# Performance work log

Measured on AMD Instinct MI355X. Metric: run time of the kernel, lower is better.

The kernel has to match this reference:

```python
import jax, jax.numpy as jnp
import numpy as np

NUM_HEADS = 12


def setup_inputs() -> dict:
    key = jax.random.key(0)
    ks = jax.random.split(key, 6)
    B, N, C = 2, 1569, 768  # N = 1 + num_frames * seq_len = 1 + 8*196
    s = 0.02
    return {
        "x": jax.random.normal(ks[0], (B, N, C), jnp.float32),
        "W_qkv": jax.random.normal(ks[1], (C, 3 * C), jnp.float32) * s,
        "W_pq": jax.random.normal(ks[2], (C, C), jnp.float32) * s,
        "W_pkv": jax.random.normal(ks[3], (C, 2 * C), jnp.float32) * s,
        "W_proj": jax.random.normal(ks[4], (C, C), jnp.float32) * s,
        "b_proj": jax.random.normal(ks[5], (C,), jnp.float32) * s,
        "seq_len": 196,
        "num_frames": 8,
    }


def reference(x, W_qkv, W_pq, W_pkv, W_proj, b_proj, seq_len, num_frames):
    h = NUM_HEADS
    B, N, C = x.shape
    d = C // h
    P, F = seq_len, num_frames  # N == 1 + F*P
    S = F * P
    scale = d ** (-0.5)

    # qkv projection (no bias), split heads -> (B*h, N, d)
    qkv = x @ W_qkv
    q, k, v = jnp.split(qkv, 3, axis=-1)

    def heads(t):
        return t.reshape(B, N, h, d).transpose(0, 2, 1, 3).reshape(B * h, N, d)

    q, k, v = map(heads, (q, k, v))

    # --- CLS token: plain attention over all tokens ---
    cls_sim = jnp.einsum('bid,bjd->bij', q[:, :1] * scale, k)  # (B*h,1,N)
    cls_attn = jax.nn.softmax(cls_sim, axis=-1)
    cls_out = jnp.einsum('bij,bjd->bid', cls_attn, v)  # (B*h,1,d)
    cls_out = cls_out.reshape(B, h, 1, d).transpose(0, 2, 1, 3).reshape(B, 1, C)

    # --- Stage 1: space attention (softmax over patches n within each frame f) ---
    q_, k_, v_ = q[:, 1:], k[:, 1:], v[:, 1:]  # (B*h, S, d)
    q_dot_k = jnp.einsum('bqd,bnd->bqn', q_, k_).reshape(B * h, S, F, P)
    space_attn = jax.nn.softmax(scale * q_dot_k, axis=-1)  # (B*h, S, F, P)
    v4 = v_.reshape(B * h, F, P, d)
    traj = jnp.einsum('bqfn,bfnd->bqfd', space_attn, v4)  # (B*h, S, F, d)
    # merge heads into channels: (B, S, F, C)
    traj = traj.reshape(B, h, S, F, d).transpose(0, 2, 3, 1, 4).reshape(B, S, F, C)

    # --- Diagonal gather: token s=f*P+n takes its own-frame trajectory f ---
    fidx = jnp.repeat(jnp.arange(F), P)  # (S,)
    x_diag = jnp.take_along_axis(traj, fidx[None, :, None, None], axis=2)[:, :, 0, :]  # (B,S,C)

    # --- Stage 2: temporal attention over frames f ---
    q2 = (x_diag @ W_pq).reshape(B, S, h, d).transpose(0, 2, 1, 3) * scale  # (B,h,S,d)
    kv2 = traj @ W_pkv  # (B,S,F,2C)
    k2, v2 = jnp.split(kv2, 2, axis=-1)

    def heads5(t):  # (B,S,F,C) -> (B,h,S,F,d)
        return t.reshape(B, S, F, h, d).transpose(0, 3, 1, 2, 4)

    k2 = heads5(k2)
    attn = jax.nn.softmax(jnp.einsum('bhsd,bhsfd->bhsf', q2, k2), axis=-1)  # (B,h,S,F)
    # use_original_code=True: values are the trajectory tensor itself, not v2
    xv = heads5(traj)
    out = jnp.einsum('bhsf,bhsfd->bhsd', attn, xv)  # (B,h,S,d)
    out = out.transpose(0, 2, 1, 3).reshape(B, S, C)

    out = jnp.concatenate([cls_out, out], axis=1) @ W_proj + b_proj  # (B,N,C)
    return out, attn
```

## Files before the change

### kernel.cpp

```cpp
#include <hip/hip_runtime.h>

#define B_ 2
#define N_ 1569
#define C_ 768
#define H_ 12
#define D_ 64
#define P_ 196
#define F_ 8
#define S_ 1568
#define QKVLD 2304
#define SCALE 0.125f

typedef unsigned short ushort_t;
using short8 = __attribute__((ext_vector_type(8))) short;
using f32x4  = __attribute__((ext_vector_type(4))) float;

__device__ __forceinline__ ushort_t f2bf(float x) {
    unsigned u = __float_as_uint(x);
    u += 0x7fffu + ((u >> 16) & 1);
    return (ushort_t)(u >> 16);
}
__device__ __forceinline__ float bf2f(ushort_t h) {
    return __uint_as_float((unsigned)h << 16);
}
__device__ __forceinline__ uint2 pack4(float a, float b, float c, float d) {
    uint2 o;
    o.x = f2bf(a) | ((unsigned)f2bf(b) << 16);
    o.y = f2bf(c) | ((unsigned)f2bf(d) << 16);
    return o;
}

__global__ __launch_bounds__(256)
void cvt_f32_bf16(const float* __restrict__ s, ushort_t* __restrict__ d, int n4)
{
    int i = blockIdx.x * 256 + threadIdx.x;
    if (i < n4) {
        float4 v = ((const float4*)s)[i];
        ((uint2*)d)[i] = pack4(v.x, v.y, v.z, v.w);
    }
}

__global__ __launch_bounds__(256)
void transpose_cvt(const float* __restrict__ src, ushort_t* __restrict__ dst,
                   int K, int ldsrc)
{
    __shared__ float tle[32][33];
    const int n0 = blockIdx.x * 32, k0 = blockIdx.y * 32;
    const int tx = threadIdx.x & 31, ty = threadIdx.x >> 5;
#pragma unroll
    for (int j = 0; j < 4; j++)
        tle[ty + 8 * j][tx] = src[(long)(k0 + ty + 8 * j) * ldsrc + n0 + tx];
    __syncthreads();
#pragma unroll
    for (int j = 0; j < 4; j++)
        dst[(long)(n0 + ty + 8 * j) * K + k0 + tx] = f2bf(tle[tx][ty + 8 * j]);
}

template<int GATHER, int OUTBF>
__global__ __launch_bounds__(256)
void gemm_bf16(const ushort_t* __restrict__ A, const ushort_t* __restrict__ Bt,
               void* __restrict__ Cv, int M, int Nn, int K,
               float alpha, const float* __restrict__ bias)
{
    __shared__ ushort_t As[128][32];
    __shared__ ushort_t Bs[128][32];

    const int tid = threadIdx.x;

    const int nwg = gridDim.x;
    const int GY  = Nn >> 7;
    const int bid = blockIdx.x;
    const int qch = nwg >> 3, rch = nwg & 7;
    const int xcd = bid & 7, lidx = bid >> 3;
    const int wg = (xcd < rch ? xcd * (qch + 1)
                              : rch * (qch + 1) + (xcd - rch) * qch) + lidx;
    const int m0 = (wg / GY) * 128, n0 = (wg % GY) * 128;

    const int wave = tid >> 6, lane = tid & 63;
    const int wm = (wave & 1) * 64, wn = (wave >> 1) * 64;
    const int lrow = lane & 15, quad = lane >> 4;

    const int srow = tid >> 2, sseg = tid & 3;
    const int wseg = sseg ^ ((srow >> 1) & 3);
    int ma0 = m0 + srow;      if (ma0 >= M) ma0 = M - 1;
    int ma1 = m0 + 64 + srow; if (ma1 >= M) ma1 = M - 1;
    long ra0, ra1;
    if (GATHER) {
        ra0 = (long)ma0 * F_ + (ma0 % S_) / P_;
        ra1 = (long)ma1 * F_ + (ma1 % S_) / P_;
    } else { ra0 = ma0; ra1 = ma1; }
    const ushort_t* ap0 = A + ra0 * K + sseg * 8;
    const ushort_t* ap1 = A + ra1 * K + sseg * 8;
    const ushort_t* bp0 = Bt + (long)(n0 + srow) * K + sseg * 8;
    const ushort_t* bp1 = Bt + (long)(n0 + 64 + srow) * K + sseg * 8;

    f32x4 acc[4][4];
#pragma unroll
    for (int i = 0; i < 4; i++)
#pragma unroll
        for (int j = 0; j < 4; j++) acc[i][j] = (f32x4){0.f, 0.f, 0.f, 0.f};

    const int rchunk = (quad ^ ((lrow >> 1) & 3)) * 8;

    uint4 aV0 = *(const uint4*)ap0;
    uint4 aV1 = *(const uint4*)ap1;
    uint4 bV0 = *(const uint4*)bp0;
    uint4 bV1 = *(const uint4*)bp1;

    const int nk = K >> 5;
    for (int kt = 0; kt < nk; kt++) {
        __syncthreads();
        *(uint4*)&As[srow][wseg * 8]      = aV0;
        *(uint4*)&As[64 + srow][wseg * 8] = aV1;
        *(uint4*)&Bs[srow][wseg * 8]      = bV0;
        *(uint4*)&Bs[64 + srow][wseg * 8] = bV1;
        __syncthreads();
        if (kt + 1 < nk) {
            int k0 = (kt + 1) * 32;
            aV0 = *(const uint4*)(ap0 + k0);
            aV1 = *(const uint4*)(ap1 + k0);
            bV0 = *(const uint4*)(bp0 + k0);
            bV1 = *(const uint4*)(bp1 + k0);
        }
        short8 af[4], bf[4];
#pragma unroll
        for (int mt = 0; mt < 4; mt++)
            af[mt] = *(const short8*)&As[wm + mt * 16 + lrow][rchunk];
#pragma unroll
        for (int nt = 0; nt < 4; nt++)
            bf[nt] = *(const short8*)&Bs[wn + nt * 16 + lrow][rchunk];
#pragma unroll
        for (int mt = 0; mt < 4; mt++)
#pragma unroll
            for (int nt = 0; nt < 4; nt++)
                acc[mt][nt] = __builtin_amdgcn_mfma_f32_16x16x32_bf16(
                    af[mt], bf[nt], acc[mt][nt], 0, 0, 0);
    }

#pragma unroll
    for (int mt = 0; mt < 4; mt++) {
#pragma unroll
        for (int nt = 0; nt < 4; nt++) {
            int row = m0 + wm + mt * 16 + quad * 4;
            int col = n0 + wn + nt * 16 + lrow;
            float bv = bias ? bias[col] : 0.f;
#pragma unroll
            for (int r = 0; r < 4; r++) {
                if (row + r < M) {
                    float v = acc[mt][nt][r] * alpha + bv;
                    if (OUTBF)
                        ((ushort_t*)Cv)[(long)(row + r) * Nn + col] = f2bf(v);
                    else
                        ((float*)Cv)[(long)(row + r) * Nn + col] = v;
                }
            }
        }
    }
}

__global__ __launch_bounds__(256)
void prep_kv(const float* __restrict__ qkv, ushort_t* __restrict__ q_bf,
             ushort_t* __restrict__ k_bf, ushort_t* __restrict__ vT_bf)
{
    const int f = blockIdx.x, h = blockIdx.y, b = blockIdx.z;
    const int t = threadIdx.x;
    const long rowbase = (long)(b * N_ + 1 + f * P_) * QKVLD;

    {
        ushort_t* qd = q_bf + ((long)(b * H_ + h) * S_ + f * P_) * 64;
        for (int u = t; u < P_ * 16; u += 256) {
            int row = u >> 4, seg = u & 15;
            float4 v = *(const float4*)(qkv + rowbase + (long)row * QKVLD + h * 64 + seg * 4);
            *(uint2*)(qd + (long)row * 64 + seg * 4) = pack4(v.x, v.y, v.z, v.w);
        }
    }
    {
        ushort_t* kd = k_bf + (long)((b * H_ + h) * F_ + f) * 13312;
        for (int u = t; u < 208 * 16; u += 256) {
            int key = u >> 4, seg = u & 15;
            float4 v = make_float4(0.f, 0.f, 0.f, 0.f);
            if (key < P_)
                v = *(const float4*)(qkv + rowbase + (long)key * QKVLD + 768 + h * 64 + seg * 4);
            int ks = seg >> 3, qq = (seg >> 1) & 3, j0 = (seg & 1) * 4;
            int nt = key >> 4, lr = key & 15;
            *(uint2*)(kd + ((ks * 13 + nt) * 64 + qq * 16 + lr) * 8 + j0)
                = pack4(v.x, v.y, v.z, v.w);
        }
    }
    __shared__ float Vl[224][68];
    for (int u = t; u < 224 * 16; u += 256) {
        int key = u >> 4, seg = u & 15;
        float4 v = make_float4(0.f, 0.f, 0.f, 0.f);
        if (key < P_)
            v = *(const float4*)(qkv + rowbase + (long)key * QKVLD + 1536 + h * 64 + seg * 4);
        *(float4*)&Vl[key][seg * 4] = v;
    }
    __syncthreads();
    {
        ushort_t* vd = vT_bf + (long)((b * H_ + h) * F_ + f) * 14336;
        for (int u = t; u < 64 * 56; u += 256) {
            int d = u / 56, kb = u % 56;
            int s = kb >> 3, qq = (kb >> 1) & 3, j0 = (kb & 1) * 4;
            int nt = d >> 4, lr = d & 15;
            *(uint2*)(vd + ((s * 4 + nt) * 64 + qq * 16 + lr) * 8 + j0) =
                pack4(Vl[kb*4+0][d], Vl[kb*4+1][d], Vl[kb*4+2][d], Vl[kb*4+3][d]);
        }
    }
}

__global__ __launch_bounds__(256)
void traj_attn_mfma(const ushort_t* __restrict__ q_bf,
                    const ushort_t* __restrict__ k_bf,
                    const ushort_t* __restrict__ vT_bf,
                    ushort_t* __restrict__ traj)
{
    __shared__ __align__(16) ushort_t Pl[4][7 * 512];

    const int t = threadIdx.x;
    const int wave = t >> 6, lane = t & 63;
    const int lrow = lane & 15, quad = lane >> 4;
    const int qt = blockIdx.x, h = blockIdx.y, b = blockIdx.z;
    const int s0 = qt * 64;
    const bool v12 = (lrow < 4);

    int qrow = s0 + wave * 16 + lrow; if (qrow > S_ - 1) qrow = S_ - 1;
    const ushort_t* qp = q_bf + ((long)(b * H_ + h) * S_ + qrow) * 64 + quad * 8;
    short8 a0 = *(const short8*)qp;
    short8 a1 = *(const short8*)(qp + 32);

    *(uint2*)&Pl[wave][6 * 512 + 256 + lane * 4] = (uint2){0, 0};

    const ushort_t* kfb = k_bf  + (long)((b * H_ + h) * F_) * 13312;
    const ushort_t* vfb = vT_bf + (long)((b * H_ + h) * F_) * 14336;

#pragma unroll 1
    for (int f = 0; f < F_; f++) {
        const ushort_t* kf = kfb + (long)f * 13312;
        const ushort_t* vf = vfb + (long)f * 14336;

        f32x4 acc[13];
#pragma unroll
        for (int nt = 0; nt < 13; nt++) acc[nt] = (f32x4){0.f, 0.f, 0.f, 0.f};
#pragma unroll
        for (int nt = 0; nt < 13; nt++) {
            short8 bv = *(const short8*)(kf + (long)nt * 512 + lane * 8);
            acc[nt] = __builtin_amdgcn_mfma_f32_16x16x32_bf16(a0, bv, acc[nt], 0, 0, 0);
        }
#pragma unroll
        for (int nt = 0; nt < 13; nt++) {
            short8 bv = *(const short8*)(kf + (long)(13 + nt) * 512 + lane * 8);
            acc[nt] = __builtin_amdgcn_mfma_f32_16x16x32_bf16(a1, bv, acc[nt], 0, 0, 0);
        }

        float rl[4];
#pragma unroll
        for (int r = 0; r < 4; r++) {
            float mx = acc[0][r];
#pragma unroll
            for (int nt = 1; nt < 12; nt++) mx = fmaxf(mx, acc[nt][r]);
            if (v12) mx = fmaxf(mx, acc[12][r]);
#pragma unroll
            for (int off = 1; off < 16; off <<= 1)
                mx = fmaxf(mx, __shfl_xor(mx, off, 16));
            float sum = 0.f;
#pragma unroll
            for (int nt = 0; nt < 12; nt++) {
                float w = __expf((acc[nt][r] - mx) * SCALE);
                acc[nt][r] = w; sum += w;
            }
            {
                float w = v12 ? __expf((acc[12][r] - mx) * SCALE) : 0.f;
                acc[12][r] = w; sum += w;
            }
#pragma unroll
            for (int off = 1; off < 16; off <<= 1)
                sum += __shfl_xor(sum, off, 16);
            rl[r] = 1.f / sum;
        }

#pragma unroll
        for (int nt = 0; nt < 13; nt++) {
            int key = nt * 16 + lrow;
            int base = (key >> 5) * 512 + ((key >> 3) & 3) * 128 + (key & 7) + quad * 32;
#pragma unroll
            for (int r = 0; r < 4; r++)
                Pl[wave][base + r * 8] = f2bf(acc[nt][r]);
        }
        asm volatile("s_waitcnt lgkmcnt(0)" ::: "memory");

        f32x4 av[4];
#pragma unroll
        for (int nt = 0; nt < 4; nt++) av[nt] = (f32x4){0.f, 0.f, 0.f, 0.f};
#pragma unroll
        for (int s = 0; s < 7; s++) {
            short8 af = *(const short8*)&Pl[wave][s * 512 + lane * 8];
#pragma unroll
            for (int nt = 0; nt < 4; nt++) {
                short8 bv = *(const short8*)(vf + (long)(s * 4 + nt) * 512 + lane * 8);
                av[nt] = __builtin_amdgcn_mfma_f32_16x16x32_bf16(af, bv, av[nt], 0, 0, 0);
            }
        }

#pragma unroll
        for (int nt = 0; nt < 4; nt++)
#pragma unroll
            for (int r = 0; r < 4; r++) {
                int so = s0 + wave * 16 + quad * 4 + r;
                if (so < S_)
                    traj[((long)(b * S_ + so) * F_ + f) * C_ + h * 64 + nt * 16 + lrow]
                        = f2bf(av[nt][r] * rl[r]);
            }
    }
}

#define CLS_CH 13
__global__ __launch_bounds__(256)
void cls_attn_part(const float* __restrict__ qkv, float* __restrict__ part)
{
    const int c = blockIdx.x, hh = blockIdx.y, b = blockIdx.z;
    const int t = threadIdx.x;
    const int n0 = c * 128;
    const int nk = (N_ - n0 < 128) ? (N_ - n0) : 128;

    __shared__ float qs[64];
    __shared__ float sc[128];
    __shared__ float red[256];

    if (t < 64) qs[t] = qkv[(long)(b * N_) * QKVLD + hh * 64 + t];
    __syncthreads();

    if (t < 128) {
        float acc = -1e30f;
        if (t < nk) {
            const float* krow = qkv + (long)(b * N_ + n0 + t) * QKVLD + 768 + hh * 64;
            acc = 0.f;
#pragma unroll
            for (int j4 = 0; j4 < 16; j4++) {
                float4 kv = *(const float4*)(krow + j4 * 4);
                acc = fmaf(kv.x, qs[j4*4+0], acc);
                acc = fmaf(kv.y, qs[j4*4+1], acc);
                acc = fmaf(kv.z, qs[j4*4+2], acc);
                acc = fmaf(kv.w, qs[j4*4+3], acc);
            }
            acc *= SCALE;
        }
        sc[t] = acc;
        red[t] = acc;
    }
    __syncthreads();
    for (int s = 64; s > 0; s >>= 1) {
        if (t < s && t + s < 128) red[t] = fmaxf(red[t], red[t + s]);
        __syncthreads();
    }
    const float m = red[0];
    __syncthreads();

    if (t < 128) {
        float w = (t < nk) ? __expf(sc[t] - m) : 0.f;
        sc[t] = w;
        red[t] = w;
    }
    __syncthreads();
    for (int s = 64; s > 0; s >>= 1) {
        if (t < s && t + s < 128) red[t] += red[t + s];
        __syncthreads();
    }
    const float lsum = red[0];
    __syncthreads();

    const int j = t & 63, grp = t >> 6;
    float acc = 0.f;
    for (int n = grp; n < nk; n += 4)
        acc = fmaf(sc[n], qkv[(long)(b * N_ + n0 + n) * QKVLD + 1536 + hh * 64 + j], acc);
    red[t] = acc;
    __syncthreads();

    float* pp = part + (long)(((b * H_ + hh) * CLS_CH) + c) * 68;
    if (t < 64)
        pp[2 + t] = red[t] + red[64 + t] + red[128 + t] + red[192 + t];
    if (t == 0) { pp[0] = m; pp[1] = lsum; }
}

__global__ __launch_bounds__(64)
void cls_attn_merge(const float* __restrict__ part, float* __restrict__ outcat)
{
    const int bh = blockIdx.x;
    const int b = bh / H_, hh = bh % H_;
    const int t = threadIdx.x;
    const float* pp = part + (long)(bh * CLS_CH) * 68;

    float m = -1e30f;
#pragma unroll
    for (int c = 0; c < CLS_CH; c++) m = fmaxf(m, pp[c * 68]);
    float l = 0.f, o = 0.f;
#pragma unroll
    for (int c = 0; c < CLS_CH; c++) {
        float w = __expf(pp[c * 68] - m);
        l = fmaf(pp[c * 68 + 1], w, l);
        o = fmaf(pp[c * 68 + 2 + t], w, o);
    }
    outcat[(long)(b * N_) * C_ + hh * 64 + t] = o / l;
}

__global__ __launch_bounds__(256)
void attn2_kernel(const float* __restrict__ q2, const ushort_t* __restrict__ k2,
                  const ushort_t* __restrict__ traj, float* __restrict__ outcat,
                  float* __restrict__ attn_out)
{
    const int bs = blockIdx.x;
    const int b = bs / S_, s = bs % S_;
    __shared__ float qs[768];
    __shared__ ushort_t ks[8 * 768];
    __shared__ float logit[12][8];
    __shared__ float wsm[12][8];
    const int t = threadIdx.x;

    const float* qrow = q2 + (long)bs * 768;
    if (t < 192) *(float4*)&qs[t * 4] = *(const float4*)(qrow + t * 4);
    const uint4* krow = (const uint4*)(k2 + (long)bs * 6144);
#pragma unroll
    for (int u = t; u < 768; u += 256)
        *(uint4*)&ks[u * 8] = krow[u];
    __syncthreads();

    if (t < 96) {
        int hh = t >> 3, f = t & 7;
        float acc = 0.f;
#pragma unroll 8
        for (int j = 0; j < 64; j++)
            acc = fmaf(qs[hh * 64 + j], bf2f(ks[f * 768 + hh * 64 + j]), acc);
        logit[hh][f] = acc;
    }
    __syncthreads();
    if (t < 12) {
        float m = logit[t][0];
#pragma unroll
        for (int f = 1; f < 8; f++) m = fmaxf(m, logit[t][f]);
        float w[8], sum = 0.f;
#pragma unroll
        for (int f = 0; f < 8; f++) { w[f] = __expf(logit[t][f] - m); sum += w[f]; }
        float r = 1.f / sum;
#pragma unroll
        for (int f = 0; f < 8; f++) wsm[t][f] = w[f] * r;
    }
    __syncthreads();
    if (t < 96) {
        int hh = t >> 3, f = t & 7;
        attn_out[((long)(b * H_ + hh) * S_ + s) * 8 + f] = wsm[hh][f];
    }
    if (t < 96) {
        const int c0 = t * 8, hh = t >> 3;
        const ushort_t* trow = traj + (long)bs * 6144;
        float o[8];
#pragma unroll
        for (int i = 0; i < 8; i++) o[i] = 0.f;
#pragma unroll
        for (int f = 0; f < 8; f++) {
            uint4 tv = *(const uint4*)(trow + f * 768 + c0);
            float wv = wsm[hh][f];
            const ushort_t* e = (const ushort_t*)&tv;
#pragma unroll
            for (int i = 0; i < 8; i++) o[i] = fmaf(wv, bf2f(e[i]), o[i]);
        }
        float* orow = outcat + ((long)(b * N_) + 1 + s) * 768 + c0;
        *(float4*)orow       = make_float4(o[0], o[1], o[2], o[3]);
        *(float4*)(orow + 4) = make_float4(o[4], o[5], o[6], o[7]);
    }
}

extern "C" void kernel_launch(void* const* d_in, const int* in_sizes, int n_in,
                              void* d_out, int out_size, void* d_ws, size_t ws_size,
                              hipStream_t stream)
{
    (void)in_sizes; (void)n_in; (void)out_size; (void)ws_size;
    const float* x     = (const float*)d_in[0];
    const float* Wqkv  = (const float*)d_in[1];
    const float* Wpq   = (const float*)d_in[2];
    const float* Wpkv  = (const float*)d_in[3];
    const float* Wproj = (const float*)d_in[4];
    const float* bproj = (const float*)d_in[5];
    float* out = (float*)d_out;

    char* p = (char*)d_ws;
    float*    qkv     = (float*)p;
    ushort_t* traj_bf = (ushort_t*)p;
    p += (size_t)25088 * 768 * 2;
    float* q2 = (float*)p;  p += (size_t)3136 * 768 * 4;
    char* c0 = p;
    ushort_t* k2_bf = (ushort_t*)c0;
    ushort_t* x_bf  = (ushort_t*)c0;
    ushort_t* q_bf  = (ushort_t*)(c0 + (size_t)4819968);
    ushort_t* k_bf  = (ushort_t*)(c0 + (size_t)4819968 + 4816896);
    ushort_t* vT_bf = (ushort_t*)(c0 + (size_t)4819968 + 4816896 + 5111808);
    p += (size_t)25088 * 768 * 2;
    float*    outcat    = (float*)p;     p += (size_t)3138 * 768 * 4;
    ushort_t* outcat_bf = (ushort_t*)p;  p += (size_t)3138 * 768 * 2;
    ushort_t* Wqkv_t  = (ushort_t*)p;    p += (size_t)1769472 * 2;
    ushort_t* Wpq_t   = (ushort_t*)p;    p += (size_t)589824 * 2;
    ushort_t* Wpkv_t  = (ushort_t*)p;    p += (size_t)589824 * 2;
    ushort_t* Wproj_t = (ushort_t*)p;    p += (size_t)589824 * 2;
    float*    cls_part = (float*)p;      p += (size_t)24 * CLS_CH * 68 * 4;
    float* attn_out = out + (size_t)3138 * 768;

    cvt_f32_bf16<<<2354, 256, 0, stream>>>(x, x_bf, 602496);
    transpose_cvt<<<dim3(72, 24), 256, 0, stream>>>(Wqkv,  Wqkv_t,  768, 2304);
    transpose_cvt<<<dim3(24, 24), 256, 0, stream>>>(Wpq,   Wpq_t,   768, 768);
    transpose_cvt<<<dim3(24, 24), 256, 0, stream>>>(Wpkv,  Wpkv_t,  768, 1536);
    transpose_cvt<<<dim3(24, 24), 256, 0, stream>>>(Wproj, Wproj_t, 768, 768);

    gemm_bf16<0, 0><<<450, 256, 0, stream>>>(x_bf, Wqkv_t, qkv, 3138, 2304, 768, 1.f, nullptr);
    prep_kv<<<dim3(8, 12, 2), 256, 0, stream>>>(qkv, q_bf, k_bf, vT_bf);
    cls_attn_part<<<dim3(CLS_CH, 12, 2), 256, 0, stream>>>(qkv, cls_part);
    cls_attn_merge<<<24, 64, 0, stream>>>(cls_part, outcat);
    traj_attn_mfma<<<dim3(25, 12, 2), 256, 0, stream>>>(q_bf, k_bf, vT_bf, traj_bf);
    gemm_bf16<1, 0><<<150, 256, 0, stream>>>(traj_bf, Wpq_t, q2, 3136, 768, 768, SCALE, nullptr);
    gemm_bf16<0, 1><<<1176, 256, 0, stream>>>(traj_bf, Wpkv_t, k2_bf, 25088, 768, 768, 1.f, nullptr);
    attn2_kernel<<<3136, 256, 0, stream>>>(q2, k2_bf, traj_bf, outcat, attn_out);
    cvt_f32_bf16<<<2354, 256, 0, stream>>>(outcat, outcat_bf, 602496);
    gemm_bf16<0, 0><<<150, 256, 0, stream>>>(outcat_bf, Wproj_t, out, 3138, 768, 768, 1.f, bproj);
}
```

Measured before the change: 329.8 us.

## Double-buffer LDS tiles and widen GEMM K-step to 64

The bf16 GEMM now uses ping-pong shared-memory buffers and a K tile of 64 instead of 32. This halves the number of K iterations and drops one of the two __syncthreads per iteration. The LDS swizzle is reworked for 128-byte rows. The cost is doubled LDS use (64 KB per block) and more prefetch registers, which may lower occupancy.

Result: slower. 493.6 us (+49.7%).

```diff
diff --git a/kernel.cpp b/kernel.cpp
--- a/kernel.cpp
+++ b/kernel.cpp
@@ -62,8 +62,8 @@
                void* __restrict__ Cv, int M, int Nn, int K,
                float alpha, const float* __restrict__ bias)
 {
-    __shared__ ushort_t As[128][32];
-    __shared__ ushort_t Bs[128][32];
+    __shared__ ushort_t As[2][128][64];
+    __shared__ ushort_t Bs[2][128][64];
 
     const int tid = threadIdx.x;
 
@@ -80,19 +80,20 @@
     const int wm = (wave & 1) * 64, wn = (wave >> 1) * 64;
     const int lrow = lane & 15, quad = lane >> 4;
 
-    const int srow = tid >> 2, sseg = tid & 3;
-    const int wseg = sseg ^ ((srow >> 1) & 3);
-    int ma0 = m0 + srow;      if (ma0 >= M) ma0 = M - 1;
-    int ma1 = m0 + 64 + srow; if (ma1 >= M) ma1 = M - 1;
-    long ra0, ra1;
-    if (GATHER) {
-        ra0 = (long)ma0 * F_ + (ma0 % S_) / P_;
-        ra1 = (long)ma1 * F_ + (ma1 % S_) / P_;
-    } else { ra0 = ma0; ra1 = ma1; }
-    const ushort_t* ap0 = A + ra0 * K + sseg * 8;
-    const ushort_t* ap1 = A + ra1 * K + sseg * 8;
-    const ushort_t* bp0 = Bt + (long)(n0 + srow) * K + sseg * 8;
-    const ushort_t* bp1 = Bt + (long)(n0 + 64 + srow) * K + sseg * 8;
+    const int srow = tid >> 3, sseg = tid & 7;
+    const int wseg = sseg ^ (srow & 7);
+
+    const ushort_t* apg[4];
+    const ushort_t* bpg[4];
+#pragma unroll
+    for (int i = 0; i < 4; i++) {
+        int ma = m0 + srow + i * 32; if (ma >= M) ma = M - 1;
+        long ra;
+        if (GATHER) ra = (long)ma * F_ + (ma % S_) / P_;
+        else        ra = ma;
+        apg[i] = A + ra * K + sseg * 8;
+        bpg[i] = Bt + (long)(n0 + srow + i * 32) * K + sseg * 8;
+    }
 
     f32x4 acc[4][4];
 #pragma unroll
@@ -100,41 +101,46 @@
 #pragma unroll
         for (int j = 0; j < 4; j++) acc[i][j] = (f32x4){0.f, 0.f, 0.f, 0.f};
 
-    const int rchunk = (quad ^ ((lrow >> 1) & 3)) * 8;
-
-    uint4 aV0 = *(const uint4*)ap0;
-    uint4 aV1 = *(const uint4*)ap1;
-    uint4 bV0 = *(const uint4*)bp0;
-    uint4 bV1 = *(const uint4*)bp1;
-
-    const int nk = K >> 5;
+    const int rkey = lrow & 7;
+
+    uint4 aV[4], bV[4];
+#pragma unroll
+    for (int i = 0; i < 4; i++) { aV[i] = *(const uint4*)apg[i]; bV[i] = *(const uint4*)bpg[i]; }
+
+    const int nk = K >> 6;
     for (int kt = 0; kt < nk; kt++) {
-        __syncthreads();
-        *(uint4*)&As[srow][wseg * 8]      = aV0;
-        *(uint4*)&As[64 + srow][wseg * 8] = aV1;
-        *(uint4*)&Bs[srow][wseg * 8]      = bV0;
-        *(uint4*)&Bs[64 + srow][wseg * 8] = bV1;
+        const int cur = kt & 1;
+#pragma unroll
+        for (int i = 0; i < 4; i++) {
+            *(uint4*)&As[cur][srow + i * 32][wseg * 8] = aV[i];
+            *(uint4*)&Bs[cur][srow + i * 32][wseg * 8] = bV[i];
+        }
         __syncthreads();
         if (kt + 1 < nk) {
-            int k0 = (kt + 1) * 32;
-            aV0 = *(const uint4*)(ap0 + k0);
-            aV1 = *(const uint4*)(ap1 + k0);
-            bV0 = *(const uint4*)(bp0 + k0);
-            bV1 = *(const uint4*)(bp1 + k0);
-        }
-        short8 af[4], bf[4];
-#pragma unroll
-        for (int mt = 0; mt < 4; mt++)
-            af[mt] = *(const short8*)&As[wm + mt * 16 + lrow][rchunk];
-#pragma unroll
-        for (int nt = 0; nt < 4; nt++)
-            bf[nt] = *(const short8*)&Bs[wn + nt * 16 + lrow][rchunk];
-#pragma unroll
-        for (int mt = 0; mt < 4; mt++)
+            const int k0 = (kt + 1) * 64;
+#pragma unroll
+            for (int i = 0; i < 4; i++) {
+                aV[i] = *(const uint4*)(apg[i] + k0);
+                bV[i] = *(const uint4*)(bpg[i] + k0);
+            }
+        }
+#pragma unroll
+        for (int kh = 0; kh < 2; kh++) {
+            short8 af[4], bf[4];
+            const int c = ((kh << 2) + quad) ^ rkey;
+#pragma unroll
+            for (int mt = 0; mt < 4; mt++)
+                af[mt] = *(const short8*)&As[cur][wm + mt * 16 + lrow][c * 8];
 #pragma unroll
             for (int nt = 0; nt < 4; nt++)
-                acc[mt][nt] = __builtin_amdgcn_mfma_f32_16x16x32_bf16(
-                    af[mt], bf[nt], acc[mt][nt], 0, 0, 0);
+                bf[nt] = *(const short8*)&Bs[cur][wn + nt * 16 + lrow][c * 8];
+#pragma unroll
+            for (int mt = 0; mt < 4; mt++)
+#pragma unroll
+                for (int nt = 0; nt < 4; nt++)
+                    acc[mt][nt] = __builtin_amdgcn_mfma_f32_16x16x32_bf16(
+                        af[mt], bf[nt], acc[mt][nt], 0, 0, 0);
+        }
     }
 
 #pragma unroll
```

## Reassociate temporal keys: project queries through W_pk instead of projecting all trajectories

Applied to the files above, without the earlier changes.

Instead of computing k2 = traj @ W_pk for all 25088 trajectory rows, the code computes per-head g_h = q2_h @ W_pk_h^T (3136x12x768) and then takes logits as dot products of g_h with the raw trajectory rows. This replaces the large 25088x768x768 GEMM with a K=64 per-head GEMM, and the attention kernel now stages traj in shared memory and reuses it for both the logits and the weighted sum. q2 is stored in bf16, and the work is split into two batch halves so the g buffer fits in the workspace. The logit dot products grow from 64 to 768 elements per (head, frame) pair, which adds arithmetic and shared-memory traffic inside the attention kernel.

Measured after the change: 325.7 us. No clear change (-1.2%).

```diff
diff --git a/kernel.cpp b/kernel.cpp
--- a/kernel.cpp
+++ b/kernel.cpp
@@ -41,6 +41,17 @@
 }
 
 __global__ __launch_bounds__(256)
+void cvt_wpk(const float* __restrict__ src, ushort_t* __restrict__ dst)
+{
+    int i = blockIdx.x * 256 + threadIdx.x;
+    if (i < 147456) {
+        int row = i / 192, c4 = i % 192;
+        float4 v = *(const float4*)(src + (long)row * 1536 + c4 * 4);
+        ((uint2*)dst)[row * 192 + c4] = pack4(v.x, v.y, v.z, v.w);
+    }
+}
+
+__global__ __launch_bounds__(256)
 void transpose_cvt(const float* __restrict__ src, ushort_t* __restrict__ dst,
                    int K, int ldsrc)
 {
@@ -62,8 +73,8 @@
                void* __restrict__ Cv, int M, int Nn, int K,
                float alpha, const float* __restrict__ bias)
 {
-    __shared__ ushort_t As[128][32];
-    __shared__ ushort_t Bs[128][32];
+    __shared__ __align__(16) ushort_t As[128][32];
+    __shared__ __align__(16) ushort_t Bs[128][32];
 
     const int tid = threadIdx.x;
 
@@ -159,6 +170,84 @@
 }
 
 __global__ __launch_bounds__(256)
+void gh_gemm(const ushort_t* __restrict__ q2bf, const ushort_t* __restrict__ Wpk,
+             ushort_t* __restrict__ gh, int row0, int nrows)
+{
+    __shared__ __align__(16) ushort_t As[128][32];
+    __shared__ __align__(16) ushort_t Bs[128][32];
+
+    const int tid = threadIdx.x;
+    const int m0 = blockIdx.x * 128, n0 = blockIdx.y * 128, h = blockIdx.z;
+    const int wave = tid >> 6, lane = tid & 63;
+    const int wm = (wave & 1) * 64, wn = (wave >> 1) * 64;
+    const int lrow = lane & 15, quad = lane >> 4;
+
+    const int srow = tid >> 2, sseg = tid & 3;
+    const int wseg = sseg ^ ((srow >> 1) & 3);
+    int ma0 = m0 + srow;      if (ma0 >= nrows) ma0 = nrows - 1;
+    int ma1 = m0 + 64 + srow; if (ma1 >= nrows) ma1 = nrows - 1;
+    const ushort_t* ap0 = q2bf + (long)(row0 + ma0) * 768 + h * 64 + sseg * 8;
+    const ushort_t* ap1 = q2bf + (long)(row0 + ma1) * 768 + h * 64 + sseg * 8;
+    const ushort_t* bp0 = Wpk + (long)(n0 + srow) * 768 + h * 64 + sseg * 8;
+    const ushort_t* bp1 = Wpk + (long)(n0 + 64 + srow) * 768 + h * 64 + sseg * 8;
+
+    f32x4 acc[4][4];
+#pragma unroll
+    for (int i = 0; i < 4; i++)
+#pragma unroll
+        for (int j = 0; j < 4; j++) acc[i][j] = (f32x4){0.f, 0.f, 0.f, 0.f};
+
+    const int rchunk = (quad ^ ((lrow >> 1) & 3)) * 8;
+
+    uint4 aV0 = *(const uint4*)ap0;
+    uint4 aV1 = *(const uint4*)ap1;
+    uint4 bV0 = *(const uint4*)bp0;
+    uint4 bV1 = *(const uint4*)bp1;
+
+#pragma unroll
+    for (int kt = 0; kt < 2; kt++) {
+        __syncthreads();
+        *(uint4*)&As[srow][wseg * 8]      = aV0;
+        *(uint4*)&As[64 + srow][wseg * 8] = aV1;
+        *(uint4*)&Bs[srow][wseg * 8]      = bV0;
+        *(uint4*)&Bs[64 + srow][wseg * 8] = bV1;
+        __syncthreads();
+        if (kt == 0) {
+            aV0 = *(const uint4*)(ap0 + 32);
+            aV1 = *(const uint4*)(ap1 + 32);
+            bV0 = *(const uint4*)(bp0 + 32);
+            bV1 = *(const uint4*)(bp1 + 32);
+        }
+        short8 af[4], bf[4];
+#pragma unroll
+        for (int mt = 0; mt < 4; mt++)
+            af[mt] = *(const short8*)&As[wm + mt * 16 + lrow][rchunk];
+#pragma unroll
+        for (int nt = 0; nt < 4; nt++)
+            bf[nt] = *(const short8*)&Bs[wn + nt * 16 + lrow][rchunk];
+#pragma unroll
+        for (int mt = 0; mt < 4; mt++)
+#pragma unroll
+            for (int nt = 0; nt < 4; nt++)
+                acc[mt][nt] = __builtin_amdgcn_mfma_f32_16x16x32_bf16(
+                    af[mt], bf[nt], acc[mt][nt], 0, 0, 0);
+    }
+
+#pragma unroll
+    for (int mt = 0; mt < 4; mt++) {
+#pragma unroll
+        for (int nt = 0; nt < 4; nt++) {
+            int row = m0 + wm + mt * 16 + quad * 4;
+            int col = n0 + wn + nt * 16 + lrow;
+#pragma unroll
+            for (int r = 0; r < 4; r++)
+                if (row + r < nrows)
+                    gh[((long)(row + r) * 12 + h) * 768 + col] = f2bf(acc[mt][nt][r]);
+        }
+    }
+}
+
+__global__ __launch_bounds__(256)
 void prep_kv(const float* __restrict__ qkv, ushort_t* __restrict__ q_bf,
              ushort_t* __restrict__ k_bf, ushort_t* __restrict__ vT_bf)
 {
@@ -403,33 +492,47 @@
 }
 
 __global__ __launch_bounds__(256)
-void attn2_kernel(const float* __restrict__ q2, const ushort_t* __restrict__ k2,
-                  const ushort_t* __restrict__ traj, float* __restrict__ outcat,
-                  float* __restrict__ attn_out)
-{
-    const int bs = blockIdx.x;
+void attn2_kernel(const ushort_t* __restrict__ gh, const ushort_t* __restrict__ traj,
+                  float* __restrict__ outcat, float* __restrict__ attn_out, int bs0)
+{
+    const int g = blockIdx.x;
+    const int bs = bs0 + g;
     const int b = bs / S_, s = bs % S_;
-    __shared__ float qs[768];
-    __shared__ ushort_t ks[8 * 768];
+    __shared__ __align__(16) ushort_t gs[12 * 776];
+    __shared__ __align__(16) ushort_t tr[8 * 776];
     __shared__ float logit[12][8];
     __shared__ float wsm[12][8];
     const int t = threadIdx.x;
 
-    const float* qrow = q2 + (long)bs * 768;
-    if (t < 192) *(float4*)&qs[t * 4] = *(const float4*)(qrow + t * 4);
-    const uint4* krow = (const uint4*)(k2 + (long)bs * 6144);
-#pragma unroll
-    for (int u = t; u < 768; u += 256)
-        *(uint4*)&ks[u * 8] = krow[u];
-    __syncthreads();
-
-    if (t < 96) {
-        int hh = t >> 3, f = t & 7;
+    const uint4* grow = (const uint4*)(gh + (long)g * 9216);
+    for (int u = t; u < 1152; u += 256) {
+        int hh = u / 96, off = u % 96;
+        *((uint4*)(gs + (size_t)hh * 776) + off) = grow[u];
+    }
+    const uint4* trow = (const uint4*)(traj + (long)bs * 6144);
+    for (int u = t; u < 768; u += 256) {
+        int f = u / 96, off = u % 96;
+        *((uint4*)(tr + (size_t)f * 776) + off) = trow[u];
+    }
+    __syncthreads();
+
+    if (t < 192) {
+        const int pair = t >> 1, half = t & 1;
+        const int hh = pair >> 3, f = pair & 7;
+        const ushort_t* gp = gs + hh * 776 + half * 384;
+        const ushort_t* tp = tr + f * 776 + half * 384;
         float acc = 0.f;
-#pragma unroll 8
-        for (int j = 0; j < 64; j++)
-            acc = fmaf(qs[hh * 64 + j], bf2f(ks[f * 768 + hh * 64 + j]), acc);
-        logit[hh][f] = acc;
+        for (int e = 0; e < 384; e += 8) {
+            uint4 gv = *(const uint4*)(gp + e);
+            uint4 tv = *(const uint4*)(tp + e);
+            const ushort_t* ge = (const ushort_t*)&gv;
+            const ushort_t* te = (const ushort_t*)&tv;
+#pragma unroll
+            for (int i = 0; i < 8; i++)
+                acc = fmaf(bf2f(ge[i]), bf2f(te[i]), acc);
+        }
+        acc += __shfl_xor(acc, 1);
+        if (half == 0) logit[hh][f] = acc;
     }
     __syncthreads();
     if (t < 12) {
@@ -450,13 +553,12 @@
     }
     if (t < 96) {
         const int c0 = t * 8, hh = t >> 3;
-        const ushort_t* trow = traj + (long)bs * 6144;
         float o[8];
 #pragma unroll
         for (int i = 0; i < 8; i++) o[i] = 0.f;
 #pragma unroll
         for (int f = 0; f < 8; f++) {
-            uint4 tv = *(const uint4*)(trow + f * 768 + c0);
+            uint4 tv = *(const uint4*)(tr + f * 776 + c0);
             float wv = wsm[hh][f];
             const ushort_t* e = (const ushort_t*)&tv;
 #pragma unroll
@@ -485,9 +587,9 @@
     float*    qkv     = (float*)p;
     ushort_t* traj_bf = (ushort_t*)p;
     p += (size_t)25088 * 768 * 2;
-    float* q2 = (float*)p;  p += (size_t)3136 * 768 * 4;
+    ushort_t* q2_bf = (ushort_t*)p;  p += (size_t)3136 * 768 * 4;
     char* c0 = p;
-    ushort_t* k2_bf = (ushort_t*)c0;
+    ushort_t* gh    = (ushort_t*)c0;
     ushort_t* x_bf  = (ushort_t*)c0;
     ushort_t* q_bf  = (ushort_t*)(c0 + (size_t)4819968);
     ushort_t* k_bf  = (ushort_t*)(c0 + (size_t)4819968 + 4816896);
@@ -497,7 +599,7 @@
     ushort_t* outcat_bf = (ushort_t*)p;  p += (size_t)3138 * 768 * 2;
     ushort_t* Wqkv_t  = (ushort_t*)p;    p += (size_t)1769472 * 2;
     ushort_t* Wpq_t   = (ushort_t*)p;    p += (size_t)589824 * 2;
-    ushort_t* Wpkv_t  = (ushort_t*)p;    p += (size_t)589824 * 2;
+    ushort_t* Wpk_bf  = (ushort_t*)p;    p += (size_t)589824 * 2;
     ushort_t* Wproj_t = (ushort_t*)p;    p += (size_t)589824 * 2;
     float*    cls_part = (float*)p;      p += (size_t)24 * CLS_CH * 68 * 4;
     float* attn_out = out + (size_t)3138 * 768;
@@ -505,7 +607,7 @@
     cvt_f32_bf16<<<2354, 256, 0, stream>>>(x, x_bf, 602496);
     transpose_cvt<<<dim3(72, 24), 256, 0, stream>>>(Wqkv,  Wqkv_t,  768, 2304);
     transpose_cvt<<<dim3(24, 24), 256, 0, stream>>>(Wpq,   Wpq_t,   768, 768);
-    transpose_cvt<<<dim3(24, 24), 256, 0, stream>>>(Wpkv,  Wpkv_t,  768, 1536);
+    cvt_wpk<<<576, 256, 0, stream>>>(Wpkv, Wpk_bf);
     transpose_cvt<<<dim3(24, 24), 256, 0, stream>>>(Wproj, Wproj_t, 768, 768);
 
     gemm_bf16<0, 0><<<450, 256, 0, stream>>>(x_bf, Wqkv_t, qkv, 3138, 2304, 768, 1.f, nullptr);
@@ -513,9 +615,11 @@
     cls_attn_part<<<dim3(CLS_CH, 12, 2), 256, 0, stream>>>(qkv, cls_part);
     cls_attn_merge<<<24, 64, 0, stream>>>(cls_part, outcat);
     traj_attn_mfma<<<dim3(25, 12, 2), 256, 0, stream>>>(q_bf, k_bf, vT_bf, traj_bf);
-    gemm_bf16<1, 0><<<150, 256, 0, stream>>>(traj_bf, Wpq_t, q2, 3136, 768, 768, SCALE, nullptr);
-    gemm_bf16<0, 1><<<1176, 256, 0, stream>>>(traj_bf, Wpkv_t, k2_bf, 25088, 768, 768, 1.f, nullptr);
-    attn2_kernel<<<3136, 256, 0, stream>>>(q2, k2_bf, traj_bf, outcat, attn_out);
+    gemm_bf16<1, 1><<<150, 256, 0, stream>>>(traj_bf, Wpq_t, q2_bf, 3136, 768, 768, SCALE, nullptr);
+    gh_gemm<<<dim3(13, 6, 12), 256, 0, stream>>>(q2_bf, Wpk_bf, gh, 0, 1568);
+    attn2_kernel<<<1568, 256, 0, stream>>>(gh, traj_bf, outcat, attn_out, 0);
+    gh_gemm<<<dim3(13, 6, 12), 256, 0, stream>>>(q2_bf, Wpk_bf, gh, 1568, 1568);
+    attn2_kernel<<<1568, 256, 0, stream>>>(gh, traj_bf, outcat, attn_out, 1568);
     cvt_f32_bf16<<<2354, 256, 0, stream>>>(outcat, outcat_bf, 602496);
     gemm_bf16<0, 0><<<150, 256, 0, stream>>>(outcat_bf, Wproj_t, out, 3138, 768, 768, 1.f, bproj);
 }
```
